# Kernel tuning notes

Measured on AMD Instinct MI355X. Metric: run time of the kernel, lower is better.

## Reference

```python
import jax, jax.numpy as jnp
import numpy as np
import math

VOCAB = 128
READ_DIM = 128
LOGIT_SCALE = 1.0 / 16.0
NUM_FF = 6
CARRY_DIM = 896
D_MODEL = CARRY_DIM + READ_DIM


def ste_sign(x):
    # forward of the STE sign: +-1, zero -> +1
    return jnp.where(x >= 0, 1.0, -1.0).astype(x.dtype)


def ste_round(x):
    return jnp.round(x)


def setup_inputs() -> dict:
    key = jax.random.key(0)
    k_tok, k_init, k_emb, k_ff, k_head, k_thr = jax.random.split(key, 6)
    tokens = jax.random.randint(k_tok, (64, 512), 0, VOCAB, dtype=jnp.int64) if jax.config.read('jax_enable_x64') else jax.random.randint(k_tok, (64, 512), 0, VOCAB, dtype=jnp.int32)
    initial_lat = jax.random.uniform(k_init, (D_MODEL,), minval=-1.0, maxval=1.0)
    embed_lat = jax.random.uniform(k_emb, (VOCAB, READ_DIM), minval=-1.0, maxval=1.0)
    ff_lat = jax.random.uniform(k_ff, (NUM_FF, D_MODEL, D_MODEL), minval=-1.0, maxval=1.0)
    head_lat = jax.random.uniform(k_head, (READ_DIM, VOCAB), minval=-1.0, maxval=1.0)
    ff_thresh_lat = jax.random.uniform(k_thr, (NUM_FF, D_MODEL), minval=-2.0, maxval=2.0)
    return {
        'tokens': tokens,
        'initial_lat': initial_lat,
        'embed_lat': embed_lat,
        'ff_lat': ff_lat,
        'head_lat': head_lat,
        'ff_thresh_lat': ff_thresh_lat,
    }


def reference(tokens, initial_lat, embed_lat, ff_lat, head_lat, ff_thresh_lat):
    B, T = tokens.shape
    num_ff = ff_lat.shape[0]
    d_model = initial_lat.shape[0]
    carry_dim = d_model - READ_DIM
    act_scale = math.sqrt(d_model)

    initial = ste_sign(initial_lat)          # [d_model]
    embed = ste_sign(embed_lat)              # [VOCAB, read_dim]
    ff = ste_sign(ff_lat)                    # [num_ff, d_model, d_model]
    head = ste_sign(head_lat)                # [read_dim, VOCAB]
    thr = ste_round(ff_thresh_lat)           # [num_ff, d_model]

    x0 = jnp.broadcast_to(initial[None, :], (B, d_model))

    def step(x, tok_t):
        # tok_t: [B]
        h = x
        for i in range(num_ff):
            pre = h @ ff[i]                  # [B, d_model]
            h = ste_sign((pre - thr[i]) / act_scale)
        carry = h[:, :carry_dim]
        read = h[:, carry_dim:]
        logits = read @ head * LOGIT_SCALE   # [B, VOCAB]
        logp = jax.nn.log_softmax(logits, axis=-1)
        loss_t = -jnp.mean(jnp.take_along_axis(logp, tok_t[:, None], axis=1))
        x_new = jnp.concatenate([carry, embed[tok_t]], axis=1)
        return x_new, loss_t

    _, losses = jax.lax.scan(step, x0, tokens.T)  # scan over T
    return jnp.mean(losses)
```

## Files before the change

### kernel.cpp

```cpp
#include <hip/hip_runtime.h>
#include <stdint.h>

typedef unsigned long long u64;
typedef u64 u64x2 __attribute__((ext_vector_type(2)));

#define VOCAB 128
#define RD 128
#define DM 1024
#define NFF 6
#define BATCH 64
#define TSTEPS 512
#define THR 256

#define OFF_EB    786432
#define OFF_HB    788480
#define OFF_LOSS  790528

__global__ void pack_ff(const float* __restrict__ ff, u64* __restrict__ ffs) {
    int wid  = blockIdx.x * (blockDim.x >> 6) + (threadIdx.x >> 6);
    int lane = threadIdx.x & 63;
    int jt = wid & 15;
    int w  = (wid >> 4) & 15;
    int L  = wid >> 8;
    int j  = jt * 64 + lane;
    const float* src = ff + ((size_t)(L * DM) + w * 64) * DM + j;
    u64 word = 0;
#pragma unroll
    for (int b = 0; b < 64; ++b) {
        float v = src[(size_t)b * DM];
        word |= (u64)(v < 0.0f) << b;
    }
    int c = j >> 8, tid = j & 255, i = w >> 1, s = w & 1;
    ffs[((((L * 4 + c) * 8 + i) * 256 + tid) << 1) + s] = word;
}

__global__ void pack_small(const float* __restrict__ emb, const float* __restrict__ head,
                           u64* __restrict__ eb, u64* __restrict__ hb) {
    int tid = threadIdx.x;
    if (tid < 128) {
        int v = tid;
        for (int wd = 0; wd < 2; ++wd) {
            u64 word = 0;
            for (int l = 0; l < 64; ++l)
                word |= (u64)(emb[v * RD + wd * 64 + l] < 0.0f) << l;
            eb[v * 2 + wd] = word;
        }
    } else {
        int v = tid - 128;
        for (int wd = 0; wd < 2; ++wd) {
            u64 word = 0;
            for (int l = 0; l < 64; ++l)
                word |= (u64)(head[(wd * 64 + l) * VOCAB + v] < 0.0f) << l;
            hb[v * 2 + wd] = word;
        }
    }
}

__global__ void
__attribute__((amdgpu_flat_work_group_size(THR, THR), amdgpu_waves_per_eu(1, 1)))
brnn_main(const int* __restrict__ tokens,
          const float* __restrict__ initial_lat,
          const float* __restrict__ thr_lat,
          const u64* __restrict__ ffs,
          const u64* __restrict__ eb,
          const u64* __restrict__ hb,
          double* __restrict__ losses)
{
    const int b    = blockIdx.x;
    const int tid  = threadIdx.x;
    const int lane = tid & 63;
    const int wv   = tid >> 6;

    __shared__ __align__(16) u64 wlds[8][1024][2];
    __shared__ __align__(16) u64 hx[2][16];
    __shared__ u64 hbL[2 * VOCAB];

    const u64x2* wsrc = (const u64x2*)ffs;

#pragma unroll
    for (int c = 0; c < 4; ++c)
#pragma unroll
        for (int i = 0; i < 8; ++i) {
            u64x2 v = wsrc[((5 * 4 + c) * 8 + i) * 256 + tid];
            wlds[i][c * 256 + tid][0] = v.x;
            wlds[i][c * 256 + tid][1] = v.y;
        }

    int cthr[NFF][4];
#pragma unroll
    for (int L = 0; L < NFF; ++L)
#pragma unroll
        for (int c = 0; c < 4; ++c) {
            int th = (int)rintf(thr_lat[L * DM + c * 256 + tid]);
            cthr[L][c] = ((DM - th) >> 1) + 1;
        }

    if (tid < 2 * VOCAB) hbL[tid] = hb[tid];

#pragma unroll
    for (int c = 0; c < 4; ++c) {
        u64 m = __ballot(initial_lat[c * 256 + tid] < 0.0f);
        if (lane == 0) hx[0][c * 4 + wv] = m;
    }
    __syncthreads();

    const int* toks = tokens + b * TSTEPS;
    double lacc = 0.0;

    for (int t = 0; t < TSTEPS; ++t) {
        int tok = toks[t];

        u64 enew = 0;
        if (wv == 0 && lane < 2) enew = eb[tok * 2 + lane];

        int p = 0;
        for (int L = 0; L < 5; ++L) {
            const ulonglong2* hp = (const ulonglong2*)hx[p];
#pragma unroll
            for (int c = 0; c < 4; ++c) {
                const u64x2* src = wsrc + ((L * 4 + c) * 8) * 256 + tid;
                u64x2 w0 = src[0 * 256], w1 = src[1 * 256], w2 = src[2 * 256],
                      w3 = src[3 * 256], w4 = src[4 * 256], w5 = src[5 * 256],
                      w6 = src[6 * 256], w7 = src[7 * 256];
                int acc = 0;
                ulonglong2 hv;
                hv = hp[0]; acc += __popcll(hv.x ^ w0.x) + __popcll(hv.y ^ w0.y);
                hv = hp[1]; acc += __popcll(hv.x ^ w1.x) + __popcll(hv.y ^ w1.y);
                hv = hp[2]; acc += __popcll(hv.x ^ w2.x) + __popcll(hv.y ^ w2.y);
                hv = hp[3]; acc += __popcll(hv.x ^ w3.x) + __popcll(hv.y ^ w3.y);
                hv = hp[4]; acc += __popcll(hv.x ^ w4.x) + __popcll(hv.y ^ w4.y);
                hv = hp[5]; acc += __popcll(hv.x ^ w5.x) + __popcll(hv.y ^ w5.y);
                hv = hp[6]; acc += __popcll(hv.x ^ w6.x) + __popcll(hv.y ^ w6.y);
                hv = hp[7]; acc += __popcll(hv.x ^ w7.x) + __popcll(hv.y ^ w7.y);
                u64 m = __ballot(acc >= cthr[L][c]);
                if (lane == 0) hx[p ^ 1][c * 4 + wv] = m;
            }
            __syncthreads();
            p ^= 1;
        }

        {
            const ulonglong2* hp = (const ulonglong2*)hx[p];
#pragma unroll
            for (int c = 0; c < 4; ++c) {
                int acc = 0;
#pragma unroll
                for (int q = 0; q < 8; ++q) {
                    ulonglong2 hv = hp[q];
                    const ulonglong2 wq = *(const ulonglong2*)wlds[q][c * 256 + tid];
                    acc += __popcll(hv.x ^ wq.x) + __popcll(hv.y ^ wq.y);
                }
                u64 m = __ballot(acc >= cthr[5][c]);
                if (lane == 0) hx[p ^ 1][c * 4 + wv] = m;
            }
            __syncthreads();
            p ^= 1;
        }

        if (wv == 0) {
            u64 r0 = hx[0][14], r1 = hx[0][15];
            u64 h0a = hbL[lane * 2 + 0],        h0b = hbL[lane * 2 + 1];
            u64 h1a = hbL[(lane + 64) * 2 + 0], h1b = hbL[(lane + 64) * 2 + 1];
            int d0 = 128 - 2 * (__popcll(r0 ^ h0a) + __popcll(r1 ^ h0b));
            int d1 = 128 - 2 * (__popcll(r0 ^ h1a) + __popcll(r1 ^ h1b));
            float l0 = (float)d0 * (1.0f / 16.0f);
            float l1 = (float)d1 * (1.0f / 16.0f);
            float mx = fmaxf(l0, l1);
#pragma unroll
            for (int s = 32; s >= 1; s >>= 1) mx = fmaxf(mx, __shfl_xor(mx, s));
            float se = __expf(l0 - mx) + __expf(l1 - mx);
#pragma unroll
            for (int s = 32; s >= 1; s >>= 1) se += __shfl_xor(se, s);
            int   tl   = tok & 63;
            float la   = __shfl(l0, tl);
            float lb   = __shfl(l1, tl);
            float ltok = (tok >> 6) ? lb : la;
            lacc += (double)(mx + __logf(se) - ltok);
            if (lane < 2) hx[0][14 + lane] = enew;
        }
        __syncthreads();
    }

    if (tid == 0) losses[b] = lacc;
}

__global__ void reduce_loss(const double* __restrict__ losses, float* __restrict__ out) {
    int lane = threadIdx.x;
    double v = losses[lane];
#pragma unroll
    for (int s = 32; s >= 1; s >>= 1) v += __shfl_down(v, s);
    if (lane == 0) out[0] = (float)(v * (1.0 / ((double)BATCH * (double)TSTEPS)));
}

extern "C" void kernel_launch(void* const* d_in, const int* in_sizes, int n_in,
                              void* d_out, int out_size, void* d_ws, size_t ws_size,
                              hipStream_t stream) {
    const int*   tokens  = (const int*)d_in[0];
    const float* initial = (const float*)d_in[1];
    const float* embed   = (const float*)d_in[2];
    const float* ff      = (const float*)d_in[3];
    const float* head    = (const float*)d_in[4];
    const float* thrl    = (const float*)d_in[5];

    char* ws = (char*)d_ws;
    u64*    ffs    = (u64*)ws;
    u64*    eb     = (u64*)(ws + OFF_EB);
    u64*    hb     = (u64*)(ws + OFF_HB);
    double* losses = (double*)(ws + OFF_LOSS);

    pack_ff<<<384, 256, 0, stream>>>(ff, ffs);
    pack_small<<<1, 256, 0, stream>>>(embed, head, eb, hb);
    brnn_main<<<BATCH, THR, 0, stream>>>(tokens, initial, thrl, ffs, eb, hb, losses);
    reduce_loss<<<1, 64, 0, stream>>>(losses, (float*)d_out);
}
```

Before: 6.305 ms.

## Double block width to 512 threads and software-prefetch next layer weights

Block size grows from 256 to 512 threads, so each thread computes two output columns per layer instead of four, and the packed weight layout is reindexed to match. Weights for the next layer are prefetched from global memory into registers while the current layer's popcounts run, hiding load latency behind the serial layer chain. __syncthreads is replaced by a custom barrier that waits only on LDS counters, so outstanding global prefetches are not drained at each barrier. Costs are higher register pressure from the two 16-word prefetch buffers and twice as many waves meeting at each barrier.

```diff
diff --git a/kernel.cpp b/kernel.cpp
--- a/kernel.cpp
+++ b/kernel.cpp
@@ -10,11 +10,17 @@
 #define NFF 6
 #define BATCH 64
 #define TSTEPS 512
-#define THR 256
+#define THR 512
 
 #define OFF_EB    786432
 #define OFF_HB    788480
 #define OFF_LOSS  790528
+
+#define BARRIER()                                            \
+    do {                                                     \
+        asm volatile("s_waitcnt lgkmcnt(0)" ::: "memory");   \
+        __builtin_amdgcn_s_barrier();                        \
+    } while (0)
 
 __global__ void pack_ff(const float* __restrict__ ff, u64* __restrict__ ffs) {
     int wid  = blockIdx.x * (blockDim.x >> 6) + (threadIdx.x >> 6);
@@ -30,8 +36,8 @@
         float v = src[(size_t)b * DM];
         word |= (u64)(v < 0.0f) << b;
     }
-    int c = j >> 8, tid = j & 255, i = w >> 1, s = w & 1;
-    ffs[((((L * 4 + c) * 8 + i) * 256 + tid) << 1) + s] = word;
+    int c2 = j >> 9, t = j & 511, i = w >> 1, s = w & 1;
+    ffs[((((L * 2 + c2) * 8 + i) * 512 + t) << 1) + s] = word;
 }
 
 __global__ void pack_small(const float* __restrict__ emb, const float* __restrict__ head,
@@ -56,8 +62,49 @@
     }
 }
 
+#define PF1(BUF, L, C2)                                                  \
+    do {                                                                 \
+        _Pragma("unroll")                                                \
+        for (int i_ = 0; i_ < 8; ++i_) {                                 \
+            u64x2 v_ = wsrc[((((L) * 2 + (C2)) * 8 + i_) << 9) + tid];   \
+            BUF[2 * i_] = v_.x; BUF[2 * i_ + 1] = v_.y;                  \
+        }                                                                \
+    } while (0)
+
+#define SLAYER(L, PFL)                                                   \
+    do {                                                                 \
+        const ulonglong2* hp_ = (const ulonglong2*)hx[(L) & 1];          \
+        ulonglong2 h0_ = hp_[0], h1_ = hp_[1], h2_ = hp_[2], h3_ = hp_[3], \
+                   h4_ = hp_[4], h5_ = hp_[5], h6_ = hp_[6], h7_ = hp_[7]; \
+        int a0_ = 0;                                                     \
+        a0_ += __popcll(h0_.x ^ p0[0])  + __popcll(h0_.y ^ p0[1]);       \
+        a0_ += __popcll(h1_.x ^ p0[2])  + __popcll(h1_.y ^ p0[3]);       \
+        a0_ += __popcll(h2_.x ^ p0[4])  + __popcll(h2_.y ^ p0[5]);       \
+        a0_ += __popcll(h3_.x ^ p0[6])  + __popcll(h3_.y ^ p0[7]);       \
+        a0_ += __popcll(h4_.x ^ p0[8])  + __popcll(h4_.y ^ p0[9]);       \
+        a0_ += __popcll(h5_.x ^ p0[10]) + __popcll(h5_.y ^ p0[11]);      \
+        a0_ += __popcll(h6_.x ^ p0[12]) + __popcll(h6_.y ^ p0[13]);      \
+        a0_ += __popcll(h7_.x ^ p0[14]) + __popcll(h7_.y ^ p0[15]);      \
+        PF1(p0, PFL, 0);   \
+        int a1_ = 0;                                                     \
+        a1_ += __popcll(h0_.x ^ p1[0])  + __popcll(h0_.y ^ p1[1]);       \
+        a1_ += __popcll(h1_.x ^ p1[2])  + __popcll(h1_.y ^ p1[3]);       \
+        a1_ += __popcll(h2_.x ^ p1[4])  + __popcll(h2_.y ^ p1[5]);       \
+        a1_ += __popcll(h3_.x ^ p1[6])  + __popcll(h3_.y ^ p1[7]);       \
+        a1_ += __popcll(h4_.x ^ p1[8])  + __popcll(h4_.y ^ p1[9]);       \
+        a1_ += __popcll(h5_.x ^ p1[10]) + __popcll(h5_.y ^ p1[11]);      \
+        a1_ += __popcll(h6_.x ^ p1[12]) + __popcll(h6_.y ^ p1[13]);      \
+        a1_ += __popcll(h7_.x ^ p1[14]) + __popcll(h7_.y ^ p1[15]);      \
+        PF1(p1, PFL, 1);                                                 \
+        u64 m0_ = __ballot(a0_ >= cthr[L][0]);                           \
+        u64 m1_ = __ballot(a1_ >= cthr[L][1]);                           \
+        if (lane == 0) { hx[((L) & 1) ^ 1][wv] = m0_;                    \
+                         hx[((L) & 1) ^ 1][8 + wv] = m1_; }              \
+        BARRIER();                                                       \
+    } while (0)
+
 __global__ void
-__attribute__((amdgpu_flat_work_group_size(THR, THR), amdgpu_waves_per_eu(1, 1)))
+__attribute__((amdgpu_flat_work_group_size(THR, THR), amdgpu_waves_per_eu(2, 2)))
 brnn_main(const int* __restrict__ tokens,
           const float* __restrict__ initial_lat,
           const float* __restrict__ thr_lat,
@@ -78,91 +125,73 @@
     const u64x2* wsrc = (const u64x2*)ffs;
 
 #pragma unroll
-    for (int c = 0; c < 4; ++c)
+    for (int c2 = 0; c2 < 2; ++c2)
 #pragma unroll
         for (int i = 0; i < 8; ++i) {
-            u64x2 v = wsrc[((5 * 4 + c) * 8 + i) * 256 + tid];
-            wlds[i][c * 256 + tid][0] = v.x;
-            wlds[i][c * 256 + tid][1] = v.y;
-        }
-
-    int cthr[NFF][4];
+            u64x2 v = wsrc[(((5 * 2 + c2) * 8 + i) << 9) + tid];
+            wlds[i][c2 * 512 + tid][0] = v.x;
+            wlds[i][c2 * 512 + tid][1] = v.y;
+        }
+
+    int cthr[NFF][2];
 #pragma unroll
     for (int L = 0; L < NFF; ++L)
 #pragma unroll
-        for (int c = 0; c < 4; ++c) {
-            int th = (int)rintf(thr_lat[L * DM + c * 256 + tid]);
-            cthr[L][c] = ((DM - th) >> 1) + 1;
+        for (int c2 = 0; c2 < 2; ++c2) {
+            int th = (int)rintf(thr_lat[L * DM + c2 * 512 + tid]);
+            cthr[L][c2] = ((DM - th) >> 1) + 1;
         }
 
     if (tid < 2 * VOCAB) hbL[tid] = hb[tid];
 
 #pragma unroll
-    for (int c = 0; c < 4; ++c) {
-        u64 m = __ballot(initial_lat[c * 256 + tid] < 0.0f);
-        if (lane == 0) hx[0][c * 4 + wv] = m;
-    }
+    for (int c2 = 0; c2 < 2; ++c2) {
+        u64 m = __ballot(initial_lat[c2 * 512 + tid] < 0.0f);
+        if (lane == 0) hx[0][c2 * 8 + wv] = m;
+    }
+
+    u64 p0[16], p1[16];
+    PF1(p0, 0, 0);
+    PF1(p1, 0, 1);
     __syncthreads();
 
     const int* toks = tokens + b * TSTEPS;
     double lacc = 0.0;
 
     for (int t = 0; t < TSTEPS; ++t) {
-        int tok = toks[t];
-
+        const int tok = toks[t];
         u64 enew = 0;
         if (wv == 0 && lane < 2) enew = eb[tok * 2 + lane];
 
-        int p = 0;
-        for (int L = 0; L < 5; ++L) {
-            const ulonglong2* hp = (const ulonglong2*)hx[p];
-#pragma unroll
-            for (int c = 0; c < 4; ++c) {
-                const u64x2* src = wsrc + ((L * 4 + c) * 8) * 256 + tid;
-                u64x2 w0 = src[0 * 256], w1 = src[1 * 256], w2 = src[2 * 256],
-                      w3 = src[3 * 256], w4 = src[4 * 256], w5 = src[5 * 256],
-                      w6 = src[6 * 256], w7 = src[7 * 256];
-                int acc = 0;
-                ulonglong2 hv;
-                hv = hp[0]; acc += __popcll(hv.x ^ w0.x) + __popcll(hv.y ^ w0.y);
-                hv = hp[1]; acc += __popcll(hv.x ^ w1.x) + __popcll(hv.y ^ w1.y);
-                hv = hp[2]; acc += __popcll(hv.x ^ w2.x) + __popcll(hv.y ^ w2.y);
-                hv = hp[3]; acc += __popcll(hv.x ^ w3.x) + __popcll(hv.y ^ w3.y);
-                hv = hp[4]; acc += __popcll(hv.x ^ w4.x) + __popcll(hv.y ^ w4.y);
-                hv = hp[5]; acc += __popcll(hv.x ^ w5.x) + __popcll(hv.y ^ w5.y);
-                hv = hp[6]; acc += __popcll(hv.x ^ w6.x) + __popcll(hv.y ^ w6.y);
-                hv = hp[7]; acc += __popcll(hv.x ^ w7.x) + __popcll(hv.y ^ w7.y);
-                u64 m = __ballot(acc >= cthr[L][c]);
-                if (lane == 0) hx[p ^ 1][c * 4 + wv] = m;
+        SLAYER(0, 1);
+        SLAYER(1, 2);
+        SLAYER(2, 3);
+        SLAYER(3, 4);
+        SLAYER(4, 0);
+
+        {
+            const ulonglong2* hp = (const ulonglong2*)hx[1];
+            int a0 = 0, a1 = 0;
+#pragma unroll
+            for (int q = 0; q < 8; ++q) {
+                ulonglong2 hv = hp[q];
+                ulonglong2 w0 = *(const ulonglong2*)wlds[q][tid];
+                ulonglong2 w1 = *(const ulonglong2*)wlds[q][512 + tid];
+                a0 += __popcll(hv.x ^ w0.x) + __popcll(hv.y ^ w0.y);
+                a1 += __popcll(hv.x ^ w1.x) + __popcll(hv.y ^ w1.y);
             }
-            __syncthreads();
-            p ^= 1;
-        }
-
-        {
-            const ulonglong2* hp = (const ulonglong2*)hx[p];
-#pragma unroll
-            for (int c = 0; c < 4; ++c) {
-                int acc = 0;
-#pragma unroll
-                for (int q = 0; q < 8; ++q) {
-                    ulonglong2 hv = hp[q];
-                    const ulonglong2 wq = *(const ulonglong2*)wlds[q][c * 256 + tid];
-                    acc += __popcll(hv.x ^ wq.x) + __popcll(hv.y ^ wq.y);
-                }
-                u64 m = __ballot(acc >= cthr[5][c]);
-                if (lane == 0) hx[p ^ 1][c * 4 + wv] = m;
-            }
-            __syncthreads();
-            p ^= 1;
+            u64 m0 = __ballot(a0 >= cthr[5][0]);
+            u64 m1 = __ballot(a1 >= cthr[5][1]);
+            if (lane == 0) { hx[0][wv] = m0; hx[0][8 + wv] = m1; }
+            BARRIER();
         }
 
         if (wv == 0) {
-            u64 r0 = hx[0][14], r1 = hx[0][15];
+            u64 ra = hx[0][14], rb = hx[0][15];
             u64 h0a = hbL[lane * 2 + 0],        h0b = hbL[lane * 2 + 1];
             u64 h1a = hbL[(lane + 64) * 2 + 0], h1b = hbL[(lane + 64) * 2 + 1];
-            int d0 = 128 - 2 * (__popcll(r0 ^ h0a) + __popcll(r1 ^ h0b));
-            int d1 = 128 - 2 * (__popcll(r0 ^ h1a) + __popcll(r1 ^ h1b));
+            int d0 = 128 - 2 * (__popcll(ra ^ h0a) + __popcll(rb ^ h0b));
+            int d1 = 128 - 2 * (__popcll(ra ^ h1a) + __popcll(rb ^ h1b));
             float l0 = (float)d0 * (1.0f / 16.0f);
             float l1 = (float)d1 * (1.0f / 16.0f);
             float mx = fmaxf(l0, l1);
@@ -178,7 +207,7 @@
             lacc += (double)(mx + __logf(se) - ltok);
             if (lane < 2) hx[0][14 + lane] = enew;
         }
-        __syncthreads();
+        BARRIER();
     }
 
     if (tid == 0) losses[b] = lacc;
```

New measurement: 5.806 ms. -7.9%, faster.

## Split block into compute and prefetch halves with async global-to-LDS weight streaming

Applied to the files above, without the earlier changes.

Raises the block to 1024 threads, one output neuron per thread, and splits the threads into two halves of 512. At each of the 12 half-layer stages one half computes popcount dot products from an LDS buffer while the other half streams the next stage's packed weights into LDS through global_load_lds. The packed weight layout is reorganized to match. This replaces direct per-thread global weight loads on the recurrence's critical path with LDS reads. In exchange, half the threads idle at every stage and each step now needs 12 barriers instead of 6.

```diff
diff --git a/kernel.cpp b/kernel.cpp
--- a/kernel.cpp
+++ b/kernel.cpp
@@ -2,7 +2,6 @@
 #include <stdint.h>
 
 typedef unsigned long long u64;
-typedef u64 u64x2 __attribute__((ext_vector_type(2)));
 
 #define VOCAB 128
 #define RD 128
@@ -10,11 +9,13 @@
 #define NFF 6
 #define BATCH 64
 #define TSTEPS 512
-#define THR 256
 
 #define OFF_EB    786432
 #define OFF_HB    788480
 #define OFF_LOSS  790528
+
+typedef const __attribute__((address_space(1))) void* gas1_t;
+typedef __attribute__((address_space(3))) void*       las3_t;
 
 __global__ void pack_ff(const float* __restrict__ ff, u64* __restrict__ ffs) {
     int wid  = blockIdx.x * (blockDim.x >> 6) + (threadIdx.x >> 6);
@@ -30,8 +31,8 @@
         float v = src[(size_t)b * DM];
         word |= (u64)(v < 0.0f) << b;
     }
-    int c = j >> 8, tid = j & 255, i = w >> 1, s = w & 1;
-    ffs[((((L * 4 + c) * 8 + i) * 256 + tid) << 1) + s] = word;
+    int half = j >> 9, c = j & 511, q = w >> 1, s = w & 1;
+    ffs[((((L * 2 + half) * 8 + q) * 512 + c) << 1) + s] = word;
 }
 
 __global__ void pack_small(const float* __restrict__ emb, const float* __restrict__ head,
@@ -56,8 +57,7 @@
     }
 }
 
-__global__ void
-__attribute__((amdgpu_flat_work_group_size(THR, THR), amdgpu_waves_per_eu(1, 1)))
+__global__ void __launch_bounds__(1024, 1)
 brnn_main(const int* __restrict__ tokens,
           const float* __restrict__ initial_lat,
           const float* __restrict__ thr_lat,
@@ -70,37 +70,35 @@
     const int tid  = threadIdx.x;
     const int lane = tid & 63;
     const int wv   = tid >> 6;
+    const int w8   = wv & 7;
+    const int half = tid >> 9;
 
-    __shared__ __align__(16) u64 wlds[8][1024][2];
+    __shared__ __align__(16) u64 wbuf[2][8][512][2];
     __shared__ __align__(16) u64 hx[2][16];
     __shared__ u64 hbL[2 * VOCAB];
 
-    const u64x2* wsrc = (const u64x2*)ffs;
-
-#pragma unroll
-    for (int c = 0; c < 4; ++c)
-#pragma unroll
-        for (int i = 0; i < 8; ++i) {
-            u64x2 v = wsrc[((5 * 4 + c) * 8 + i) * 256 + tid];
-            wlds[i][c * 256 + tid][0] = v.x;
-            wlds[i][c * 256 + tid][1] = v.y;
-        }
-
-    int cthr[NFF][4];
-#pragma unroll
-    for (int L = 0; L < NFF; ++L)
-#pragma unroll
-        for (int c = 0; c < 4; ++c) {
-            int th = (int)rintf(thr_lat[L * DM + c * 256 + tid]);
-            cthr[L][c] = ((DM - th) >> 1) + 1;
-        }
-
     if (tid < 2 * VOCAB) hbL[tid] = hb[tid];
 
+    int cthr[NFF];
 #pragma unroll
-    for (int c = 0; c < 4; ++c) {
-        u64 m = __ballot(initial_lat[c * 256 + tid] < 0.0f);
-        if (lane == 0) hx[0][c * 4 + wv] = m;
+    for (int L = 0; L < NFF; ++L) {
+        int th = (int)rintf(thr_lat[L * DM + tid]);
+        cthr[L] = ((DM - th) >> 1) + 1;
+    }
+
+    {
+        u64 m = __ballot(initial_lat[tid] < 0.0f);
+        if (lane == 0) hx[0][wv] = m;
+    }
+
+    if (half == 0) {
+#pragma unroll
+        for (int k = 0; k < 8; ++k) {
+            const u64* gp = ffs + ((size_t)(k * 512 + w8 * 64 + lane) << 1);
+            __builtin_amdgcn_global_load_lds((gas1_t)gp,
+                                             (las3_t)&wbuf[0][k][w8 * 64][0], 16, 0, 0);
+        }
+        asm volatile("s_waitcnt vmcnt(0)" ::: "memory");
     }
     __syncthreads();
 
@@ -108,69 +106,54 @@
     double lacc = 0.0;
 
     for (int t = 0; t < TSTEPS; ++t) {
-        int tok = toks[t];
-
+        const int tok = toks[t];
         u64 enew = 0;
         if (wv == 0 && lane < 2) enew = eb[tok * 2 + lane];
 
-        int p = 0;
-        for (int L = 0; L < 5; ++L) {
-            const ulonglong2* hp = (const ulonglong2*)hx[p];
 #pragma unroll
-            for (int c = 0; c < 4; ++c) {
-                const u64x2* src = wsrc + ((L * 4 + c) * 8) * 256 + tid;
-                u64x2 w0 = src[0 * 256], w1 = src[1 * 256], w2 = src[2 * 256],
-                      w3 = src[3 * 256], w4 = src[4 * 256], w5 = src[5 * 256],
-                      w6 = src[6 * 256], w7 = src[7 * 256];
-                int acc = 0;
-                ulonglong2 hv;
-                hv = hp[0]; acc += __popcll(hv.x ^ w0.x) + __popcll(hv.y ^ w0.y);
-                hv = hp[1]; acc += __popcll(hv.x ^ w1.x) + __popcll(hv.y ^ w1.y);
-                hv = hp[2]; acc += __popcll(hv.x ^ w2.x) + __popcll(hv.y ^ w2.y);
-                hv = hp[3]; acc += __popcll(hv.x ^ w3.x) + __popcll(hv.y ^ w3.y);
-                hv = hp[4]; acc += __popcll(hv.x ^ w4.x) + __popcll(hv.y ^ w4.y);
-                hv = hp[5]; acc += __popcll(hv.x ^ w5.x) + __popcll(hv.y ^ w5.y);
-                hv = hp[6]; acc += __popcll(hv.x ^ w6.x) + __popcll(hv.y ^ w6.y);
-                hv = hp[7]; acc += __popcll(hv.x ^ w7.x) + __popcll(hv.y ^ w7.y);
-                u64 m = __ballot(acc >= cthr[L][c]);
-                if (lane == 0) hx[p ^ 1][c * 4 + wv] = m;
-            }
-            __syncthreads();
-            p ^= 1;
-        }
-
-        {
-            const ulonglong2* hp = (const ulonglong2*)hx[p];
-#pragma unroll
-            for (int c = 0; c < 4; ++c) {
+        for (int s = 0; s < 12; ++s) {
+            const int L  = s >> 1, hf = s & 1;
+            const int s1 = (s + 1) % 12;
+            const int L1 = s1 >> 1, hf1 = s1 & 1;
+            if (half == hf) {
+                const ulonglong2* hp = (const ulonglong2*)hx[L & 1];
                 int acc = 0;
 #pragma unroll
                 for (int q = 0; q < 8; ++q) {
                     ulonglong2 hv = hp[q];
-                    const ulonglong2 wq = *(const ulonglong2*)wlds[q][c * 256 + tid];
-                    acc += __popcll(hv.x ^ wq.x) + __popcll(hv.y ^ wq.y);
+                    ulonglong2 w  = *(const ulonglong2*)wbuf[hf][q][tid & 511];
+                    acc += __popcll(hv.x ^ w.x) + __popcll(hv.y ^ w.y);
                 }
-                u64 m = __ballot(acc >= cthr[5][c]);
-                if (lane == 0) hx[p ^ 1][c * 4 + wv] = m;
+                u64 m = __ballot(acc >= cthr[L]);
+                if (lane == 0) hx[(L + 1) & 1][hf * 8 + w8] = m;
+            } else {
+#pragma unroll
+                for (int k = 0; k < 8; ++k) {
+                    const u64* gp = ffs +
+                        ((size_t)((((L1 * 2 + hf1) * 8 + k) * 512) + w8 * 64 + lane) << 1);
+                    __builtin_amdgcn_global_load_lds((gas1_t)gp,
+                                                     (las3_t)&wbuf[hf1][k][w8 * 64][0],
+                                                     16, 0, 0);
+                }
+                asm volatile("s_waitcnt vmcnt(0)" ::: "memory");
             }
             __syncthreads();
-            p ^= 1;
         }
 
         if (wv == 0) {
-            u64 r0 = hx[0][14], r1 = hx[0][15];
+            u64 ra = hx[0][14], rb = hx[0][15];
             u64 h0a = hbL[lane * 2 + 0],        h0b = hbL[lane * 2 + 1];
             u64 h1a = hbL[(lane + 64) * 2 + 0], h1b = hbL[(lane + 64) * 2 + 1];
-            int d0 = 128 - 2 * (__popcll(r0 ^ h0a) + __popcll(r1 ^ h0b));
-            int d1 = 128 - 2 * (__popcll(r0 ^ h1a) + __popcll(r1 ^ h1b));
+            int d0 = 128 - 2 * (__popcll(ra ^ h0a) + __popcll(rb ^ h0b));
+            int d1 = 128 - 2 * (__popcll(ra ^ h1a) + __popcll(rb ^ h1b));
             float l0 = (float)d0 * (1.0f / 16.0f);
             float l1 = (float)d1 * (1.0f / 16.0f);
             float mx = fmaxf(l0, l1);
 #pragma unroll
-            for (int s = 32; s >= 1; s >>= 1) mx = fmaxf(mx, __shfl_xor(mx, s));
+            for (int sh = 32; sh >= 1; sh >>= 1) mx = fmaxf(mx, __shfl_xor(mx, sh));
             float se = __expf(l0 - mx) + __expf(l1 - mx);
 #pragma unroll
-            for (int s = 32; s >= 1; s >>= 1) se += __shfl_xor(se, s);
+            for (int sh = 32; sh >= 1; sh >>= 1) se += __shfl_xor(se, sh);
             int   tl   = tok & 63;
             float la   = __shfl(l0, tl);
             float lb   = __shfl(l1, tl);
@@ -188,7 +171,7 @@
     int lane = threadIdx.x;
     double v = losses[lane];
 #pragma unroll
-    for (int s = 32; s >= 1; s >>= 1) v += __shfl_down(v, s);
+    for (int sh = 32; sh >= 1; sh >>= 1) v += __shfl_down(v, sh);
     if (lane == 0) out[0] = (float)(v * (1.0 / ((double)BATCH * (double)TSTEPS)));
 }
 
@@ -210,6 +193,6 @@
 
     pack_ff<<<384, 256, 0, stream>>>(ff, ffs);
     pack_small<<<1, 256, 0, stream>>>(embed, head, eb, hb);
-    brnn_main<<<BATCH, THR, 0, stream>>>(tokens, initial, thrl, ffs, eb, hb, losses);
+    brnn_main<<<BATCH, 1024, 0, stream>>>(tokens, initial, thrl, ffs, eb, hb, losses);
     reduce_loss<<<1, 64, 0, stream>>>(losses, (float*)d_out);
 }
```

Result: slower. 8.208 ms (+30.2%).
